# Performance work log

Hardware: AMD Instinct MI355X
Metric: run time of the kernel (lower is better)

## Reference

```python
import jax, jax.numpy as jnp
import numpy as np

B = 1; T = 2048; H = 2048; NH = 16; KVH = 4; HD = 128; WIN = 512; SINK = 64
S = 64; NG = 4; MLP_I = 5504; CK = 4
INTER = NH * HD; CONV_DIM = INTER + 2 * NG * S; NPROJ = INTER + CONV_DIM + NH
EPS = 1e-6; MEPS = 1e-5


def rmsnorm(x, w, eps):
    return x * jax.lax.rsqrt(jnp.mean(x * x, -1, keepdims=True) + eps) * w


def rotate_half(x):
    h = x.shape[-1] // 2
    return jnp.concatenate([-x[..., h:], x[..., :h]], -1)


def setup_inputs():
    key = jax.random.key(0)
    ks = jax.random.split(key, 32)
    rn = lambda k, s, sc=0.02: jax.random.normal(k, s, dtype=jnp.float32) * sc
    inv = 1.0 / (10000.0 ** (np.arange(0, HD, 2, dtype=np.float64) / HD))
    fr = np.outer(np.arange(T), inv)
    emb = np.concatenate([fr, fr], -1)
    return {
        'hidden_states': jax.random.normal(ks[0], (B, T, H), dtype=jnp.float32),
        'cos': jnp.asarray(np.cos(emb), jnp.float32)[None],
        'sin': jnp.asarray(np.sin(emb), jnp.float32)[None],
        'ln1_w': jnp.ones((H,), jnp.float32),
        'q_w': rn(ks[1], (NH * HD, H)), 'q_b': rn(ks[2], (NH * HD,)),
        'k_w': rn(ks[3], (KVH * HD, H)), 'k_b': rn(ks[4], (KVH * HD,)),
        'v_w': rn(ks[5], (KVH * HD, H)), 'v_b': rn(ks[6], (KVH * HD,)),
        'o_w': rn(ks[7], (H, NH * HD)),
        'in_proj_w': rn(ks[8], (NPROJ, H)),
        'conv_w': rn(ks[9], (CONV_DIM, 1, CK), 0.1),
        'conv_b': rn(ks[10], (CONV_DIM,), 0.1),
        'dt_bias': rn(ks[11], (NH,), 0.5),
        'A_log': rn(ks[12], (NH,), 0.5),
        'D': rn(ks[13], (NH,), 0.5),
        'mnorm_w': jnp.ones((INTER,), jnp.float32),
        'out_proj_w': rn(ks[14], (H, INTER)),
        'ln2_w': jnp.ones((H,), jnp.float32),
        'gate_w': rn(ks[15], (MLP_I, H)),
        'up_w': rn(ks[16], (MLP_I, H)),
        'down_w': rn(ks[17], (H, MLP_I)),
    }


def _mamba2(ev, in_proj_w, conv_w, conv_b, dt_bias, A_log, D, mnorm_w, out_proj_w):
    # ev: [B, L, H] evicted hidden states; Mamba2 with expand=1 (intermediate=INTER)
    L = ev.shape[1]
    proj = jnp.einsum('blh,ph->blp', ev, in_proj_w)
    z = proj[..., :INTER]
    xBC = proj[..., INTER:INTER + CONV_DIM]
    dt = proj[..., INTER + CONV_DIM:]
    # depthwise causal conv1d, kernel 4
    xBC = jax.lax.conv_general_dilated(
        xBC.transpose(0, 2, 1), conv_w, (1,), [(CK - 1, 0)],
        dimension_numbers=('NCH', 'OIH', 'NCH'), feature_group_count=CONV_DIM)
    xBC = jax.nn.silu((xBC + conv_b[None, :, None]).transpose(0, 2, 1))
    x = xBC[..., :INTER].reshape(B, L, NH, HD)
    Bm = jnp.repeat(xBC[..., INTER:INTER + NG * S].reshape(B, L, NG, S), NH // NG, axis=2)
    Cm = jnp.repeat(xBC[..., INTER + NG * S:].reshape(B, L, NG, S), NH // NG, axis=2)
    dt = jax.nn.softplus(dt + dt_bias)  # [B, L, NH]
    A = -jnp.exp(A_log)  # [NH]

    def scan_one(xb, bb, cb, db):
        def step(state, inp):
            xt, bt, ct, dtt = inp  # [NH,HD],[NH,S],[NH,S],[NH]
            decay = jnp.exp(dtt * A)[:, None, None]
            state = decay * state + (dtt[:, None] * xt)[..., None] * bt[:, None, :]
            y = jnp.einsum('hds,hs->hd', state, ct) + D[:, None] * xt
            return state, y
        _, ys = jax.lax.scan(step, jnp.zeros((NH, HD, S), xb.dtype), (xb, bb, cb, db))
        return ys

    y = jax.vmap(scan_one)(x, Bm, Cm, dt).reshape(B, L, INTER)
    g = y * jax.nn.silu(z)  # gated RMSNorm
    g = g * jax.lax.rsqrt(jnp.mean(g * g, -1, keepdims=True) + MEPS) * mnorm_w
    return jnp.einsum('bli,hi->blh', g, out_proj_w)


def reference(hidden_states, cos, sin, ln1_w, q_w, q_b, k_w, k_b, v_w, v_b, o_w,
              in_proj_w, conv_w, conv_b, dt_bias, A_log, D, mnorm_w, out_proj_w,
              ln2_w, gate_w, up_w, down_w):
    pre = rmsnorm(hidden_states, ln1_w, EPS)  # input_layernorm
    evict_end = T - WIN
    mem_out = _mamba2(pre[:, SINK:evict_end, :], in_proj_w, conv_w, conv_b,
                      dt_bias, A_log, D, mnorm_w, out_proj_w)  # [B, Le, H]
    mem_act = mem_out[:, -1:, :]

    def qkv(x, w, b, nh):
        return (jnp.einsum('blh,ph->blp', x, w) + b).reshape(x.shape[0], x.shape[1], nh, HD).transpose(0, 2, 1, 3)

    q = qkv(pre, q_w, q_b, NH)
    k = qkv(pre, k_w, k_b, KVH)
    v = qkv(pre, v_w, v_b, KVH)
    c = cos[:, None]; s = sin[:, None]
    q = q * c + rotate_half(q) * s
    k = k * c + rotate_half(k) * s
    # mem token injection at position SINK (mem projections are not rotated)
    q = q.at[:, :, SINK, :].set(qkv(mem_act, q_w, q_b, NH)[:, :, 0, :])
    k = k.at[:, :, SINK, :].set(qkv(mem_act, k_w, k_b, KVH)[:, :, 0, :])
    v = v.at[:, :, SINK, :].set(qkv(mem_act, v_w, v_b, KVH)[:, :, 0, :])
    # sink + sliding-window causal mask with mem-token bias
    row = jnp.arange(T)[:, None]; col = jnp.arange(T)[None, :]
    protected = SINK + 1
    bad = (col > row) | ((col < row - WIN) & (col >= protected))
    minv = jnp.finfo(jnp.float32).min
    mask = jnp.where(bad, minv, 0.0)[None, None]
    le_fact = (T - SINK - WIN) / T
    mask = mask.at[..., SINK].add(0.5 * le_fact)
    rep = NH // KVH
    kf = jnp.repeat(k, rep, axis=1)
    vf = jnp.repeat(v, rep, axis=1)
    scores = jnp.einsum('bhqd,bhkd->bhqk', q, kf) * (HD ** -0.5) + mask
    attn = jax.nn.softmax(scores, axis=-1)
    o = jnp.einsum('bhqk,bhkd->bhqd', attn, vf).transpose(0, 2, 1, 3).reshape(B, T, NH * HD)
    # training-path merge: sinks | mem_out | window
    merged = jnp.concatenate([o[:, :SINK], mem_out, o[:, T - WIN:]], axis=1)
    attn_out = jnp.einsum('blp,hp->blh', merged, o_w)
    h = hidden_states + attn_out
    m = rmsnorm(h, ln2_w, EPS)
    mlp = jnp.einsum('bli,hi->blh',
                     jax.nn.silu(jnp.einsum('blh,ih->bli', m, gate_w)) * jnp.einsum('blh,ih->bli', m, up_w),
                     down_w)
    return h + mlp
```

## Files before the change

### kernel.cpp

```cpp
#include <hip/hip_runtime.h>
#include <hip/hip_bf16.h>

#define TSEQ   2048
#define HDIM   2048
#define NHEAD  16
#define KVHEAD 4
#define HEADD  128
#define WINSZ  512
#define SINKN  64
#define MLPI   5504
#define CONVD  2560
#define NPROJD 4624
#define LMEM   1472
#define NCHUNK 23
#define QKVD   3072

typedef unsigned short bf_t;
typedef __attribute__((ext_vector_type(8))) short short8;
typedef __attribute__((ext_vector_type(4))) short s4v;
typedef __attribute__((ext_vector_type(4))) float ffrag;

#define BOF_PRE   0ull
#define BOF_QKV   8388608ull
#define BOF_P     8388608ull
// ... 27 lines not shown
typedef const __attribute__((address_space(1))) unsigned gl_u32;
typedef __attribute__((address_space(3))) unsigned lds_u32;
__device__ __forceinline__ void gld16(const void* g, void* l) {
  __builtin_amdgcn_global_load_lds((gl_u32*)g, (lds_u32*)l, 16, 0, 0);
}

__global__ void detect_k(const void* __restrict__ ln1, int* __restrict__ flag) {
  unsigned w0 = *(const unsigned*)ln1;
  *flag = (w0 == 0x3F803F80u) ? 1 : 0;
}

__global__ __launch_bounds__(256) void wconv_k(const float* __restrict__ src,
    bf_t* __restrict__ dst, int n8, const int* __restrict__ flagp) {
  if (*flagp) return;
  int idx = blockIdx.x*256 + threadIdx.x;
  if (idx >= n8) return;
  const float* s = src + (size_t)idx*8;
  float4 a = *(const float4*)s, b = *(const float4*)(s+4);
  short8 o;
  o[0]=(short)f2bf(a.x); o[1]=(short)f2bf(a.y); o[2]=(short)f2bf(a.z); o[3]=(short)f2bf(a.w);
  o[4]=(short)f2bf(b.x); o[5]=(short)f2bf(b.y); o[6]=(short)f2bf(b.z); o[7]=(short)f2bf(b.w);
  *(short8*)(dst + (size_t)idx*8) = o;
}

__global__ __launch_bounds__(256) void rms_in_k(const void* __restrict__ x,
    const void* __restrict__ w, bf_t* __restrict__ out, float eps,
    const int* __restrict__ flagp) {
  int bf = *flagp;
  int row = blockIdx.x, tid = threadIdx.x;
  float v[8];
  if (bf) {
    const bf_t* xr = (const bf_t*)x + (size_t)row*HDIM + tid*8;
#pragma unroll
    for (int j = 0; j < 8; ++j) v[j] = bf2f(xr[j]);
  } else {
    const float* xr = (const float*)x + (size_t)row*HDIM + tid*8;
    float4 a = *(const float4*)xr, b = *(const float4*)(xr+4);
    v[0]=a.x; v[1]=a.y; v[2]=a.z; v[3]=a.w; v[4]=b.x; v[5]=b.y; v[6]=b.z; v[7]=b.w;
  }
  float ss = 0.f;
#pragma unroll
  for (int j = 0; j < 8; ++j) ss += v[j]*v[j];
  __shared__ float red[256];
  red[tid] = ss; __syncthreads();
  for (int s = 128; s > 0; s >>= 1) { if (tid < s) red[tid] += red[tid+s]; __syncthreads(); }
  float scale = 1.f / sqrtf(red[0]*(1.f/HDIM) + eps);
  bf_t* o = out + (size_t)row*HDIM + tid*8;
#pragma unroll
  for (int j = 0; j < 8; ++j) o[j] = f2bf(v[j]*scale*ldin(w, tid*8+j, bf));
}

__global__ __launch_bounds__(256) void rms_f2b_k(const float* __restrict__ x,
    const void* __restrict__ w, bf_t* __restrict__ out, float eps,
    const int* __restrict__ flagp) {
  int bf = *flagp;
  int row = blockIdx.x, tid = threadIdx.x;
  const float* xr = x + (size_t)row*2048 + tid*8;
  float4 a = *(const float4*)xr, b = *(const float4*)(xr+4);
  float v[8] = {a.x,a.y,a.z,a.w,b.x,b.y,b.z,b.w};
  float ss = 0.f;
#pragma unroll
  for (int j = 0; j < 8; ++j) ss += v[j]*v[j];
  __shared__ float red[256];
  red[tid] = ss; __syncthreads();
  for (int s = 128; s > 0; s >>= 1) { if (tid < s) red[tid] += red[tid+s]; __syncthreads(); }
  float scale = 1.f / sqrtf(red[0]*(1.f/2048.f) + eps);
  bf_t* o = out + (size_t)row*2048 + tid*8;
#pragma unroll
  for (int j = 0; j < 8; ++j) o[j] = f2bf(v[j]*scale*ldin(w, tid*8+j, bf));
}

__global__ __launch_bounds__(256) void tgemm_k(
    const bf_t* __restrict__ A, int lda,
    const void* __restrict__ W0, const void* __restrict__ W1, const void* __restrict__ W2,
    const bf_t* __restrict__ C0, const bf_t* __restrict__ C1, const bf_t* __restrict__ C2,
    int ldw, int n1, int n2,
    const void* __restrict__ b0, const void* __restrict__ b1, const void* __restrict__ b2,
    const void* __restrict__ res,
    const float* __restrict__ hf,
    void* __restrict__ out,
    int ldc, int M, int N, int K, int mode, int outbf,
    const int* __restrict__ flagp) {
  int bf = *flagp;
  __shared__ short As[4096];
  __shared__ short Bs[2048];
  int tid = threadIdx.x;
  int lane = tid & 63, wv = tid >> 6;
  int bm = blockIdx.y << 7, bn = blockIdx.x << 6;

  int trow = tid >> 2;
  int kc = (tid & 3) << 3;
  int ar0 = bm + trow;        if (ar0 > M-1) ar0 = M-1;
  int ar1 = bm + 64 + trow;   if (ar1 > M-1) ar1 = M-1;
  int wr  = bn + trow;        if (wr > N-1) wr = N-1;
  const bf_t* ga0 = A + (size_t)ar0*lda + kc;
  const bf_t* ga1 = A + (size_t)ar1*lda + kc;
  const bf_t* w0 = bf ? (const bf_t*)W0 : C0;
  const bf_t* w1 = bf ? (const bf_t*)W1 : C1;
  const bf_t* w2 = bf ? (const bf_t*)W2 : C2;
  const bf_t* Wsel; int wrl;
  if (wr < n1)      { Wsel = w0; wrl = wr; }
  else if (wr < n2) { Wsel = w1; wrl = wr - n1; }
  else              { Wsel = w2; wrl = wr - n2; }
  const bf_t* gwb = Wsel + (size_t)wrl*ldw + kc;
  short* lA0 = As + wv*512;
  short* lA1 = As + 2048 + wv*512;
  short* lB  = Bs + wv*512;

  int wm = (wv & 1) << 6, wn = (wv >> 1) << 5;
  int fr = lane & 15, fq = (lane >> 4) << 3;

  ffrag acc[4][2];
#pragma unroll
  for (int i = 0; i < 4; ++i)
#pragma unroll
    for (int j = 0; j < 2; ++j) acc[i][j] = (ffrag){0.f,0.f,0.f,0.f};

  for (int k0 = 0; k0 < K; k0 += 32) {
    gld16(ga0 + k0, lA0);
    gld16(ga1 + k0, lA1);
    gld16(gwb + k0, lB);
    __syncthreads();
    short8 af[4], bfr[2];
#pragma unroll
    for (int i = 0; i < 4; ++i)
      af[i] = *(const short8*)&As[(wm + i*16 + fr)*32 + fq];
#pragma unroll
    for (int j = 0; j < 2; ++j)
      bfr[j] = *(const short8*)&Bs[(wn + j*16 + fr)*32 + fq];
#pragma unroll
    for (int i = 0; i < 4; ++i)
#pragma unroll
      for (int j = 0; j < 2; ++j)
        acc[i][j] = __builtin_amdgcn_mfma_f32_16x16x32_bf16(af[i], bfr[j], acc[i][j], 0, 0, 0);
    __syncthreads();
  }

  int rbase = (lane >> 4) << 2;
  int cbase = lane & 15;
#pragma unroll
  for (int i = 0; i < 4; ++i) {
#pragma unroll
    for (int j = 0; j < 2; ++j) {
#pragma unroll
      for (int r = 0; r < 4; ++r) {
        int m = bm + wm + i*16 + rbase + r;
        int n = bn + wn + j*16 + cbase;
        if (m >= M || n >= N) continue;
        size_t ci = (size_t)m*ldc + n;
        float v = acc[i][j][r];
        if (mode == 0) {
          if (b0) {
            if (n < n1)      v += ldin(b0, n, bf);
            else if (n < n2) v += ldin(b1, n - n1, bf);
            else             v += ldin(b2, n - n2, bf);
          }
          if (outbf) ((bf_t*)out)[ci] = f2bf(v); else ((float*)out)[ci] = v;
        } else if (mode == 1) {
          ((float*)out)[ci] = v + ldin(res, ci, bf);
        } else {
          float hv = hf[ci] + v;
          if (bf) ((bf_t*)out)[ci] = f2bf(hv); else ((float*)out)[ci] = hv;
        }
      }
    }
  }
}

__global__ __launch_bounds__(256) void fgemm_k(
    const bf_t* __restrict__ A, int lda,
    const void* __restrict__ Wg, const void* __restrict__ Wu,
    const bf_t* __restrict__ Cg, const bf_t* __restrict__ Cu, int ldw,
    bf_t* __restrict__ out, int M, int N, int K,
    const int* __restrict__ flagp) {
  int bf = *flagp;
  __shared__ short As[4096];
  __shared__ short Bs[4096];
  int tid = threadIdx.x;
  int lane = tid & 63, wv = tid >> 6;
  int bm = blockIdx.y << 7, bn = blockIdx.x << 6;

  int trow = tid >> 2;
  int kc = (tid & 3) << 3;
  int ar0 = bm + trow;        if (ar0 > M-1) ar0 = M-1;
  int ar1 = bm + 64 + trow;   if (ar1 > M-1) ar1 = M-1;
  int wr  = bn + trow;        if (wr > N-1) wr = N-1;
  const bf_t* ga0 = A + (size_t)ar0*lda + kc;
  const bf_t* ga1 = A + (size_t)ar1*lda + kc;
  const bf_t* wg = bf ? (const bf_t*)Wg : Cg;
  const bf_t* wu = bf ? (const bf_t*)Wu : Cu;
  const bf_t* gwgb = wg + (size_t)wr*ldw + kc;
  const bf_t* gwub = wu + (size_t)wr*ldw + kc;
  short* lA0 = As + wv*512;
  short* lA1 = As + 2048 + wv*512;
  short* lBg = Bs + wv*512;
  short* lBu = Bs + 2048 + wv*512;

  int wm = (wv & 1) << 6, wn = (wv >> 1) << 5;
  int fr = lane & 15, fq = (lane >> 4) << 3;

  ffrag ag[4][2], au[4][2];
#pragma unroll
  for (int i = 0; i < 4; ++i)
#pragma unroll
    for (int j = 0; j < 2; ++j) { ag[i][j] = (ffrag){0.f,0.f,0.f,0.f}; au[i][j] = (ffrag){0.f,0.f,0.f,0.f}; }

  for (int k0 = 0; k0 < K; k0 += 32) {
    gld16(ga0 + k0, lA0);
    gld16(ga1 + k0, lA1);
    gld16(gwgb + k0, lBg);
    gld16(gwub + k0, lBu);
    __syncthreads();
    short8 af[4], bg[2], bu[2];
#pragma unroll
    for (int i = 0; i < 4; ++i)
      af[i] = *(const short8*)&As[(wm + i*16 + fr)*32 + fq];
#pragma unroll
    for (int j = 0; j < 2; ++j) {
      bg[j] = *(const short8*)&Bs[(wn + j*16 + fr)*32 + fq];
      bu[j] = *(const short8*)&Bs[2048 + (wn + j*16 + fr)*32 + fq];
    }
#pragma unroll
    for (int i = 0; i < 4; ++i)
#pragma unroll
      for (int j = 0; j < 2; ++j) {
        ag[i][j] = __builtin_amdgcn_mfma_f32_16x16x32_bf16(af[i], bg[j], ag[i][j], 0, 0, 0);
        au[i][j] = __builtin_amdgcn_mfma_f32_16x16x32_bf16(af[i], bu[j], au[i][j], 0, 0, 0);
      }
    __syncthreads();
  }

  int rbase = (lane >> 4) << 2;
  int cbase = lane & 15;
#pragma unroll
  for (int i = 0; i < 4; ++i)
#pragma unroll
    for (int j = 0; j < 2; ++j)
#pragma unroll
      for (int r = 0; r < 4; ++r) {
        int m = bm + wm + i*16 + rbase + r;
        int n = bn + wn + j*16 + cbase;
        if (m >= M || n >= N) continue;
        float g = ag[i][j][r], u = au[i][j][r];
        out[(size_t)m*N + n] = f2bf(siluf(g) * u);
      }
}

__global__ __launch_bounds__(256) void rope_k(float* __restrict__ tb, int stride,
    const void* __restrict__ cosp, const void* __restrict__ sinp,
    int nheads, const int* __restrict__ flagp) {
  int bf = *flagp;
  int idx = blockIdx.x*256 + threadIdx.x;
  int d = idx & 63;
  int rem = idx >> 6;
  int tpos = rem / nheads, hh = rem % nheads;
  float* base = tb + (size_t)tpos*stride + hh*128;
  float a = base[d], b = base[d+64];
  float c0 = ldin(cosp, (size_t)tpos*128 + d, bf),    s0 = ldin(sinp, (size_t)tpos*128 + d, bf);
  float c1 = ldin(cosp, (size_t)tpos*128 + d + 64, bf), s1 = ldin(sinp, (size_t)tpos*128 + d + 64, bf);
  base[d]    = a*c0 - b*s0;
  base[d+64] = b*c1 + a*s1;
}

__global__ __launch_bounds__(256) void conv_k(const float* __restrict__ proj,
    const void* __restrict__ convw, const void* __restrict__ convb,
    float* __restrict__ xbcc, const int* __restrict__ flagp) {
  int bf = *flagp;
  int idx = blockIdx.x*256 + threadIdx.x;
  int t = idx / CONVD, c = idx % CONVD;
  float acc = ldin(convb, c, bf);
#pragma unroll
  for (int j = 0; j < 4; ++j) {
    int tt = t - 3 + j;
    if (tt >= 0) acc += ldin(convw, (size_t)c*4 + j, bf) * proj[(size_t)tt*NPROJD + 2048 + c];
  }
  xbcc[idx] = siluf(acc);
}

__global__ __launch_bounds__(256) void dt_k(const float* __restrict__ proj,
    const void* __restrict__ dtb, const void* __restrict__ alog,
    float* __restrict__ dtv, float* __restrict__ ga, const int* __restrict__ flagp) {
  int bf = *flagp;
  int idx = blockIdx.x*256 + threadIdx.x;
  int t = idx >> 4, h = idx & 15;
  float raw = proj[(size_t)t*NPROJD + 4608 + h] + ldin(dtb, h, bf);
  float dt = (raw > 30.f) ? raw : log1pf(expf(raw));
  float A = -expf(ldin(alog, h, bf));
  dtv[idx] = dt;
  ga[idx] = dt*A;
}

__global__ __launch_bounds__(256) void cums_k(const float* __restrict__ ga,
    float* __restrict__ Lc) {
  int wid = blockIdx.x*4 + (threadIdx.x >> 6);
  int lane = threadIdx.x & 63;
  int h = wid / NCHUNK, c = wid % NCHUNK;
  int t = c*64 + lane;
  float a = ga[(size_t)t*16 + h];
#pragma unroll
  for (int off = 1; off < 64; off <<= 1) {
    float o = __shfl_up(a, off, 64);
    if (lane >= off) a += o;
  }
  Lc[(size_t)(h*NCHUNK + c)*64 + lane] = a;
}

__global__ __launch_bounds__(256) void chunkstate_k(
    const float* __restrict__ xbcc, const float* __restrict__ dtv,
    const float* __restrict__ Lc, float* __restrict__ Pbuf) {
  __shared__ short XT[128*72];
  __shared__ short BT[64*72];
  __shared__ float wj[64];
  int tid = threadIdx.x, lane = tid & 63, wv = tid >> 6;
  int b = blockIdx.x;
  int h = b & 15, c = b >> 4;
  int g64 = (h >> 2) << 6;
  size_t hc = (size_t)(h*NCHUNK + c);

  if (tid < 64) {
    float L63 = Lc[hc*64 + 63];
// ... 129 lines not shown
    }
  }
  __syncthreads();

  {
    int rbase = (lane >> 4) << 2, cbase = lane & 15;
    int j = wv*16 + cbase;
#pragma unroll
    for (int i = 0; i < 4; ++i)
#pragma unroll
      for (int r = 0; r < 4; ++r) {
        int ii = i*16 + rbase + r;
        float v = (j <= ii) ? s0[i][r] * expf(Lch[ii] - Lch[j]) * dtch[j] : 0.f;
        BsS[ii*72 + j] = (short)f2bf(v);
      }
#pragma unroll
    for (int e = 0; e < 16; ++e) {
      int idx = tid*16 + e;
      int ii = idx >> 6, s = idx & 63;
      Cs[ii*72 + s] = (short)f2bf(bf2f((bf_t)Cs[ii*72 + s]) * expf(Lch[ii]));
    }
  }
  __syncthreads();

  ffrag acc[4][2];
#pragma unroll
  for (int i = 0; i < 4; ++i)
#pragma unroll
    for (int j = 0; j < 2; ++j) acc[i][j] = (ffrag){0.f,0.f,0.f,0.f};
#pragma unroll
  for (int k0 = 0; k0 < 64; k0 += 32) {
    short8 xb[2], af[4];
#pragma unroll
    for (int j = 0; j < 2; ++j)
      xb[j] = *(const short8*)&XT[(wv*32 + j*16 + fr)*72 + k0 + fq];
#pragma unroll
    for (int i = 0; i < 4; ++i)
      af[i] = *(const short8*)&BsS[(i*16 + fr)*72 + k0 + fq];
#pragma unroll
    for (int i = 0; i < 4; ++i)
#pragma unroll
      for (int j = 0; j < 2; ++j)
        acc[i][j] = __builtin_amdgcn_mfma_f32_16x16x32_bf16(af[i], xb[j], acc[i][j], 0, 0, 0);
  }
#pragma unroll
  for (int k0 = 0; k0 < 64; k0 += 32) {
    short8 sb[2], af[4];
#pragma unroll
    for (int j = 0; j < 2; ++j)
      sb[j] = *(const short8*)&Sinb[(wv*32 + j*16 + fr)*72 + k0 + fq];
#pragma unroll
    for (int i = 0; i < 4; ++i)
      af[i] = *(const short8*)&Cs[(i*16 + fr)*72 + k0 + fq];
#pragma unroll
    for (int i = 0; i < 4; ++i)
#pragma unroll
      for (int j = 0; j < 2; ++j)
        acc[i][j] = __builtin_amdgcn_mfma_f32_16x16x32_bf16(af[i], sb[j], acc[i][j], 0, 0, 0);
  }

  int rbase = (lane >> 4) << 2, cbase = lane & 15;
#pragma unroll
  for (int i = 0; i < 4; ++i)
#pragma unroll
    for (int j = 0; j < 2; ++j)
#pragma unroll
      for (int r = 0; r < 4; ++r) {
        int ii = i*16 + rbase + r;
        int d = wv*32 + j*16 + cbase;
        int t = c*64 + ii;
        int col = h*128 + d;
        float x = xbcc[(size_t)t*CONVD + col];
        float z = proj[(size_t)t*NPROJD + col];
        float y = acc[i][j][r] + Dh*x;
        g[(size_t)t*2048 + col] = y * siluf(z);
      }
}

__global__ __launch_bounds__(256) void memact_k(
    const bf_t* __restrict__ merged,
    const void* __restrict__ qw, const void* __restrict__ qb,
    const void* __restrict__ kw, const void* __restrict__ kb,
    const void* __restrict__ vw, const void* __restrict__ vb,
    float* __restrict__ qkv, const int* __restrict__ flagp) {
  int bf = *flagp;
  int p = blockIdx.x, tid = threadIdx.x;
  const bf_t* ma = merged + (size_t)1535*2048;
  const void* w; const void* b; int off;
  if (p < 2048)      { w = qw; b = qb; off = p; }
  else if (p < 2560) { w = kw; b = kb; off = p - 2048; }
  else               { w = vw; b = vb; off = p - 2560; }
  float partial = 0.f;
  size_t wbase = (size_t)off*2048;
  for (int j = tid; j < 2048; j += 256) partial += bf2f(ma[j])*ldin(w, wbase + j, bf);
  __shared__ float red[256];
  red[tid] = partial; __syncthreads();
  for (int s = 128; s > 0; s >>= 1) { if (tid < s) red[tid] += red[tid+s]; __syncthreads(); }
  if (tid == 0) qkv[(size_t)64*QKVD + p] = red[0] + ldin(b, off, bf);
}

__global__ __launch_bounds__(256) void attn3_k(
    const float* __restrict__ qkv, bf_t* __restrict__ merged) {
  __shared__ short Qs[64*136];
  __shared__ short Ks[64*136];
  __shared__ short Vt[128*72];
  __shared__ short Pb[64*72];

  int bid = blockIdx.x;
  int g = bid & 3, hg = (bid >> 2) & 3, qt = bid >> 4;
  int r0 = (qt == 0) ? 0 : (1536 + 64*(qt-1));
  int tid = threadIdx.x, lane = tid & 63, wv = tid >> 6;

  int qcol = g*512 + hg*128;
  int kcol = 2048 + g*128;
  int vcol = 2560 + g*128;

  int fr = lane & 15, fq = (lane >> 4) << 3;
  int rloc = (lane >> 4) << 2;
  int cb = lane & 15;

  {
    int row = tid >> 2, c4 = tid & 3;
    const float* qp = qkv + (size_t)(r0 + row)*QKVD + qcol;
#pragma unroll
    for (int rep = 0; rep < 8; ++rep) {
      int d = (c4 + rep*4)*4;
      float4 v = *(const float4*)(qp + d);
      s4v o;
      o[0] = (short)f2bf(v.x); o[1] = (short)f2bf(v.y);
      o[2] = (short)f2bf(v.z); o[3] = (short)f2bf(v.w);
      *(s4v*)&Qs[row*136 + d] = o;
    }
  }
  __syncthreads();

  float m4[4] = {-3.0e38f, -3.0e38f, -3.0e38f, -3.0e38f};
  float l4[4] = {0.f, 0.f, 0.f, 0.f};
  ffrag o8[8];
#pragma unroll
  for (int n = 0; n < 8; ++n) o8[n] = (ffrag){0.f,0.f,0.f,0.f};

  int ntiles = (qt == 0) ? 1 : 11;
  for (int t = 0; t < ntiles; ++t) {
    int kb = (t == 0) ? 0 : ((t == 1) ? 64 : (r0 - 512 + 64*(t-2)));

    {
      int row = tid >> 2, c4 = tid & 3;
      const float* kp = qkv + (size_t)(kb + row)*QKVD + kcol;
#pragma unroll
      for (int rep = 0; rep < 8; ++rep) {
        int d = (c4 + rep*4)*4;
        float4 v = *(const float4*)(kp + d);
        s4v o;
        o[0] = (short)f2bf(v.x); o[1] = (short)f2bf(v.y);
        o[2] = (short)f2bf(v.z); o[3] = (short)f2bf(v.w);
        *(s4v*)&Ks[row*136 + d] = o;
      }
    }
#pragma unroll
    for (int it = 0; it < 8; ++it) {
      int task = tid + it*256;
      int d = task & 127, jg = task >> 7;
      const float* vp = qkv + (size_t)(kb + jg*4)*QKVD + vcol + d;
      s4v o;
      o[0] = (short)f2bf(vp[0]);
      o[1] = (short)f2bf(vp[QKVD]);
      o[2] = (short)f2bf(vp[2*QKVD]);
      o[3] = (short)f2bf(vp[3*QKVD]);
      *(s4v*)&Vt[d*72 + jg*4] = o;
    }
    __syncthreads();

    ffrag s[4];
#pragma unroll
    for (int n = 0; n < 4; ++n) s[n] = (ffrag){0.f,0.f,0.f,0.f};
#pragma unroll
    for (int k0 = 0; k0 < 128; k0 += 32) {
// ... 41 lines not shown
#pragma unroll
      for (int rg = 0; rg < 4; ++rg) {
        float p = expf(s[n][rg] - m4[rg]);
        ts[rg] += p;
        Pb[(wv*16 + rloc + rg)*72 + n*16 + cb] = (short)f2bf(p);
      }
#pragma unroll
    for (int rg = 0; rg < 4; ++rg) {
#pragma unroll
      for (int off = 1; off < 16; off <<= 1) ts[rg] += __shfl_xor(ts[rg], off, 64);
      l4[rg] += ts[rg];
    }

#pragma unroll
    for (int k0 = 0; k0 < 64; k0 += 32) {
      short8 ap = *(const short8*)&Pb[(wv*16 + fr)*72 + k0 + fq];
#pragma unroll
      for (int n = 0; n < 8; ++n) {
        short8 bv = *(const short8*)&Vt[(n*16 + fr)*72 + k0 + fq];
        o8[n] = __builtin_amdgcn_mfma_f32_16x16x32_bf16(ap, bv, o8[n], 0, 0, 0);
      }
    }
    __syncthreads();
  }

  float inv[4];
#pragma unroll
  for (int rg = 0; rg < 4; ++rg) inv[rg] = 1.f / l4[rg];
#pragma unroll
  for (int n = 0; n < 8; ++n)
#pragma unroll
    for (int rg = 0; rg < 4; ++rg) {
      int i = wv*16 + rloc + rg;
      int d = n*16 + cb;
      merged[(size_t)(r0 + i)*2048 + (g*4 + hg)*128 + d] = f2bf(o8[n][rg]*inv[rg]);
    }
}

extern "C" void kernel_launch(void* const* d_in, const int* in_sizes, int n_in,
                              void* d_out, int out_size, void* d_ws, size_t ws_size,
                              hipStream_t stream) {
  const void* hidden = d_in[0];
  const void* cosp   = d_in[1];
  const void* sinp   = d_in[2];
  const void* ln1w   = d_in[3];
  const void* qw = d_in[4];  const void* qb = d_in[5];
  const void* kw = d_in[6];  const void* kb = d_in[7];
  const void* vw = d_in[8];  const void* vb = d_in[9];
  const void* ow = d_in[10];
  const void* inpw = d_in[11];
  const void* convw = d_in[12]; const void* convb = d_in[13];
  const void* dtb = d_in[14]; const void* alog = d_in[15]; const void* dd = d_in[16];
  const void* mnw = d_in[17]; const void* outpw = d_in[18];
  const void* ln2w = d_in[19];
  const void* gatew = d_in[20]; const void* upw = d_in[21]; const void* downw = d_in[22];

  char* wsb = (char*)d_ws;
  bf_t*  pre    = (bf_t*)(wsb + BOF_PRE);
  bf_t*  mbuf   = (bf_t*)(wsb + BOF_PRE);
  float* qkv    = (float*)(wsb + BOF_QKV);
  float* Pbuf   = (float*)(wsb + BOF_P);
  float* Sbuf   = (float*)(wsb + BOF_S);
  float* proj   = (float*)(wsb + BOF_PROJ);
  bf_t*  Gbuf   = (bf_t*)(wsb + BOF_GB);
  float* xbcc   = (float*)(wsb + BOF_XBCC);
  float* gbuf   = (float*)(wsb + BOF_GF);
  bf_t*  merged = (bf_t*)(wsb + BOF_MERG);
  bf_t*  gn     = (bf_t*)(wsb + BOF_GN);
  float* hbuf   = (float*)(wsb + BOF_H);
  float* dtv    = (float*)(wsb + BOF_DT);
  float* ga     = (float*)(wsb + BOF_GA);
  int*   flag   = (int*)(wsb + BOF_FLAG);
  float* Lc     = (float*)(wsb + BOF_LC);
  bf_t*  cvA    = (bf_t*)(wsb + BOF_CNV_A);
  bf_t*  cvB    = (bf_t*)(wsb + BOF_CNV_B);
  bf_t*  cvq    = cvB;
  bf_t*  cvk    = cvB + 4194304;
  bf_t*  cvv    = cvB + 5242880;

  detect_k<<<dim3(1), dim3(1), 0, stream>>>(ln1w, flag);
  rms_in_k<<<dim3(TSEQ), dim3(256), 0, stream>>>(hidden, ln1w, pre, 1e-6f, flag);

  wconv_k<<<dim3(4624), dim3(256), 0, stream>>>((const float*)inpw, cvA, 1183744, flag);
  tgemm_k<<<dim3(73,12), dim3(256), 0, stream>>>(pre + (size_t)64*2048, 2048,
      inpw, nullptr, nullptr, cvA, nullptr, nullptr, 2048, NPROJD, NPROJD,
      nullptr, nullptr, nullptr,
      nullptr, nullptr, proj, NPROJD, LMEM, NPROJD, 2048, 0, 0, flag);
  conv_k<<<dim3((LMEM*CONVD)/256), dim3(256), 0, stream>>>(proj, convw, convb, xbcc, flag);
  dt_k<<<dim3((LMEM*16)/256), dim3(256), 0, stream>>>(proj, dtb, alog, dtv, ga, flag);
  cums_k<<<dim3(92), dim3(256), 0, stream>>>(ga, Lc);
  chunkstate_k<<<dim3(368), dim3(256), 0, stream>>>(xbcc, dtv, Lc, Pbuf);
  statepass_k<<<dim3(512), dim3(256), 0, stream>>>(Pbuf, Lc, Sbuf);
  wconv_k<<<dim3(2048), dim3(256), 0, stream>>>((const float*)outpw, cvA, 524288, flag);
  chunkout_k<<<dim3(368), dim3(256), 0, stream>>>(xbcc, proj, dtv, Lc, Sbuf, dd, gbuf, flag);
  rms_f2b_k<<<dim3(LMEM), dim3(256), 0, stream>>>(gbuf, mnw, gn, 1e-5f, flag);
  tgemm_k<<<dim3(32,12), dim3(256), 0, stream>>>(gn, 2048,
      outpw, nullptr, nullptr, cvA, nullptr, nullptr, 2048, 2048, 2048,
      nullptr, nullptr, nullptr,
      nullptr, nullptr, merged + (size_t)64*2048, 2048, LMEM, 2048, 2048, 0, 1, flag);

  wconv_k<<<dim3(2048), dim3(256), 0, stream>>>((const float*)qw, cvq, 524288, flag);
  wconv_k<<<dim3(512),  dim3(256), 0, stream>>>((const float*)kw, cvk, 131072, flag);
  wconv_k<<<dim3(512),  dim3(256), 0, stream>>>((const float*)vw, cvv, 131072, flag);
  tgemm_k<<<dim3(48,16), dim3(256), 0, stream>>>(pre, 2048,
      qw, kw, vw, cvq, cvk, cvv, 2048, 2048, 2560, qb, kb, vb,
      nullptr, nullptr, qkv, QKVD, 2048, QKVD, 2048, 0, 0, flag);
  rope_k<<<dim3(8192), dim3(256), 0, stream>>>(qkv, QKVD, cosp, sinp, 16, flag);
  rope_k<<<dim3(2048), dim3(256), 0, stream>>>(qkv + 2048, QKVD, cosp, sinp, 4, flag);

  memact_k<<<dim3(3072), dim3(256), 0, stream>>>(merged, qw, qb, kw, kb, vw, vb, qkv, flag);
  attn3_k<<<dim3(144), dim3(256), 0, stream>>>(qkv, merged);

  wconv_k<<<dim3(2048), dim3(256), 0, stream>>>((const float*)ow, cvB, 524288, flag);
  tgemm_k<<<dim3(32,16), dim3(256), 0, stream>>>(merged, 2048,
      ow, nullptr, nullptr, cvB, nullptr, nullptr, 2048, 2048, 2048,
      nullptr, nullptr, nullptr,
      hidden, nullptr, hbuf, 2048, 2048, 2048, 2048, 1, 0, flag);
  rms_f2b_k<<<dim3(TSEQ), dim3(256), 0, stream>>>(hbuf, ln2w, mbuf, 1e-6f, flag);

  wconv_k<<<dim3(5504), dim3(256), 0, stream>>>((const float*)gatew, cvA, 1409024, flag);
  wconv_k<<<dim3(5504), dim3(256), 0, stream>>>((const float*)upw,   cvB, 1409024, flag);
  fgemm_k<<<dim3(86,16), dim3(256), 0, stream>>>(mbuf, 2048, gatew, upw, cvA, cvB, 2048,
      Gbuf, 2048, MLPI, 2048, flag);
  wconv_k<<<dim3(5504), dim3(256), 0, stream>>>((const float*)downw, cvA, 1409024, flag);
  tgemm_k<<<dim3(32,16), dim3(256), 0, stream>>>(Gbuf, MLPI,
      downw, nullptr, nullptr, cvA, nullptr, nullptr, MLPI, 2048, 2048,
      nullptr, nullptr, nullptr,
      nullptr, hbuf, d_out, 2048, 2048, 2048, MLPI, 3, 0, flag);
}
```

Baseline: 705.0 us.

## Enlarge GEMM tiles to 128x128 and 128x96 and use bf16 weights in memact

The generic GEMM's block tile grows from 128x64 to 128x128, with each wave computing a 64x64 sub-tile (4x4 MFMA fragments). The fused gate/up GEMM grows to 128x96 per block. Grid sizes shrink to match. The goal is more reuse of each loaded tile per K step and less redundant global traffic for the A operand. memact_k now reads the pre-converted bf16 weight copies instead of converting fp32 weights on the fly. The trade-offs are higher register and LDS use, lower occupancy, and fewer blocks on the smaller GEMMs, which may underfill the 256 CUs.

Measured after the change: 785.8 us. +11.5%, slower.

```diff
diff --git a/kernel.cpp b/kernel.cpp
--- a/kernel.cpp
+++ b/kernel.cpp
@@ -134,55 +134,65 @@
     const int* __restrict__ flagp) {
   int bf = *flagp;
   __shared__ short As[4096];
-  __shared__ short Bs[2048];
+  __shared__ short Bs[4096];
   int tid = threadIdx.x;
   int lane = tid & 63, wv = tid >> 6;
-  int bm = blockIdx.y << 7, bn = blockIdx.x << 6;
+  int bm = blockIdx.y << 7, bn = blockIdx.x << 7;
 
   int trow = tid >> 2;
   int kc = (tid & 3) << 3;
   int ar0 = bm + trow;        if (ar0 > M-1) ar0 = M-1;
   int ar1 = bm + 64 + trow;   if (ar1 > M-1) ar1 = M-1;
-  int wr  = bn + trow;        if (wr > N-1) wr = N-1;
+  int wr0 = bn + trow;        if (wr0 > N-1) wr0 = N-1;
+  int wr1 = bn + 64 + trow;   if (wr1 > N-1) wr1 = N-1;
   const bf_t* ga0 = A + (size_t)ar0*lda + kc;
   const bf_t* ga1 = A + (size_t)ar1*lda + kc;
   const bf_t* w0 = bf ? (const bf_t*)W0 : C0;
   const bf_t* w1 = bf ? (const bf_t*)W1 : C1;
   const bf_t* w2 = bf ? (const bf_t*)W2 : C2;
-  const bf_t* Wsel; int wrl;
-  if (wr < n1)      { Wsel = w0; wrl = wr; }
-  else if (wr < n2) { Wsel = w1; wrl = wr - n1; }
-  else              { Wsel = w2; wrl = wr - n2; }
-  const bf_t* gwb = Wsel + (size_t)wrl*ldw + kc;
+  const bf_t* gwb0; const bf_t* gwb1;
+  {
+    const bf_t* Ws; int wrl;
+    if (wr0 < n1)      { Ws = w0; wrl = wr0; }
+    else if (wr0 < n2) { Ws = w1; wrl = wr0 - n1; }
+    else               { Ws = w2; wrl = wr0 - n2; }
+    gwb0 = Ws + (size_t)wrl*ldw + kc;
+    if (wr1 < n1)      { Ws = w0; wrl = wr1; }
+    else if (wr1 < n2) { Ws = w1; wrl = wr1 - n1; }
+    else               { Ws = w2; wrl = wr1 - n2; }
+    gwb1 = Ws + (size_t)wrl*ldw + kc;
+  }
   short* lA0 = As + wv*512;
   short* lA1 = As + 2048 + wv*512;
-  short* lB  = Bs + wv*512;
-
-  int wm = (wv & 1) << 6, wn = (wv >> 1) << 5;
+  short* lB0 = Bs + wv*512;
+  short* lB1 = Bs + 2048 + wv*512;
+
+  int wm = (wv & 1) << 6, wn = (wv >> 1) << 6;
   int fr = lane & 15, fq = (lane >> 4) << 3;
 
-  ffrag acc[4][2];
+  ffrag acc[4][4];
 #pragma unroll
   for (int i = 0; i < 4; ++i)
 #pragma unroll
-    for (int j = 0; j < 2; ++j) acc[i][j] = (ffrag){0.f,0.f,0.f,0.f};
+    for (int j = 0; j < 4; ++j) acc[i][j] = (ffrag){0.f,0.f,0.f,0.f};
 
   for (int k0 = 0; k0 < K; k0 += 32) {
     gld16(ga0 + k0, lA0);
     gld16(ga1 + k0, lA1);
-    gld16(gwb + k0, lB);
+    gld16(gwb0 + k0, lB0);
+    gld16(gwb1 + k0, lB1);
     __syncthreads();
-    short8 af[4], bfr[2];
+    short8 af[4], bfr[4];
 #pragma unroll
     for (int i = 0; i < 4; ++i)
       af[i] = *(const short8*)&As[(wm + i*16 + fr)*32 + fq];
 #pragma unroll
-    for (int j = 0; j < 2; ++j)
+    for (int j = 0; j < 4; ++j)
       bfr[j] = *(const short8*)&Bs[(wn + j*16 + fr)*32 + fq];
 #pragma unroll
     for (int i = 0; i < 4; ++i)
 #pragma unroll
-      for (int j = 0; j < 2; ++j)
+      for (int j = 0; j < 4; ++j)
         acc[i][j] = __builtin_amdgcn_mfma_f32_16x16x32_bf16(af[i], bfr[j], acc[i][j], 0, 0, 0);
     __syncthreads();
   }
@@ -192,7 +202,7 @@
 #pragma unroll
   for (int i = 0; i < 4; ++i) {
 #pragma unroll
-    for (int j = 0; j < 2; ++j) {
+    for (int j = 0; j < 4; ++j) {
 #pragma unroll
       for (int r = 0; r < 4; ++r) {
         int m = bm + wm + i*16 + rbase + r;
@@ -226,55 +236,63 @@
     const int* __restrict__ flagp) {
   int bf = *flagp;
   __shared__ short As[4096];
-  __shared__ short Bs[4096];
+  __shared__ short Bs[6144];
   int tid = threadIdx.x;
   int lane = tid & 63, wv = tid >> 6;
-  int bm = blockIdx.y << 7, bn = blockIdx.x << 6;
+  int bm = blockIdx.y << 7, bn = blockIdx.x * 96;
 
   int trow = tid >> 2;
   int kc = (tid & 3) << 3;
   int ar0 = bm + trow;        if (ar0 > M-1) ar0 = M-1;
   int ar1 = bm + 64 + trow;   if (ar1 > M-1) ar1 = M-1;
-  int wr  = bn + trow;        if (wr > N-1) wr = N-1;
   const bf_t* ga0 = A + (size_t)ar0*lda + kc;
   const bf_t* ga1 = A + (size_t)ar1*lda + kc;
   const bf_t* wg = bf ? (const bf_t*)Wg : Cg;
   const bf_t* wu = bf ? (const bf_t*)Wu : Cu;
-  const bf_t* gwgb = wg + (size_t)wr*ldw + kc;
-  const bf_t* gwub = wu + (size_t)wr*ldw + kc;
+  const bf_t* gbsrc[3];
+#pragma unroll
+  for (int p = 0; p < 3; ++p) {
+    int g = p*256 + tid;
+    int isu = (g >= 384);
+    int r = isu ? ((g - 384) >> 2) : (g >> 2);
+    int col = bn + r; if (col > N-1) col = N-1;
+    gbsrc[p] = (isu ? wu : wg) + (size_t)col*ldw + ((g & 3) << 3);
+  }
   short* lA0 = As + wv*512;
   short* lA1 = As + 2048 + wv*512;
-  short* lBg = Bs + wv*512;
-  short* lBu = Bs + 2048 + wv*512;
-
-  int wm = (wv & 1) << 6, wn = (wv >> 1) << 5;
+  short* lBp0 = Bs + wv*512;
+  short* lBp1 = Bs + 2048 + wv*512;
+  short* lBp2 = Bs + 4096 + wv*512;
+
+  int wm = (wv & 1) << 6, wn = (wv >> 1) * 48;
   int fr = lane & 15, fq = (lane >> 4) << 3;
 
-  ffrag ag[4][2], au[4][2];
+  ffrag ag[4][3], au[4][3];
 #pragma unroll
   for (int i = 0; i < 4; ++i)
 #pragma unroll
-    for (int j = 0; j < 2; ++j) { ag[i][j] = (ffrag){0.f,0.f,0.f,0.f}; au[i][j] = (ffrag){0.f,0.f,0.f,0.f}; }
+    for (int j = 0; j < 3; ++j) { ag[i][j] = (ffrag){0.f,0.f,0.f,0.f}; au[i][j] = (ffrag){0.f,0.f,0.f,0.f}; }
 
   for (int k0 = 0; k0 < K; k0 += 32) {
     gld16(ga0 + k0, lA0);
     gld16(ga1 + k0, lA1);
-    gld16(gwgb + k0, lBg);
-    gld16(gwub + k0, lBu);
+    gld16(gbsrc[0] + k0, lBp0);
+    gld16(gbsrc[1] + k0, lBp1);
+    gld16(gbsrc[2] + k0, lBp2);
     __syncthreads();
-    short8 af[4], bg[2], bu[2];
+    short8 af[4], bg[3], bu[3];
 #pragma unroll
     for (int i = 0; i < 4; ++i)
       af[i] = *(const short8*)&As[(wm + i*16 + fr)*32 + fq];
 #pragma unroll
-    for (int j = 0; j < 2; ++j) {
+    for (int j = 0; j < 3; ++j) {
       bg[j] = *(const short8*)&Bs[(wn + j*16 + fr)*32 + fq];
-      bu[j] = *(const short8*)&Bs[2048 + (wn + j*16 + fr)*32 + fq];
+      bu[j] = *(const short8*)&Bs[3072 + (wn + j*16 + fr)*32 + fq];
     }
 #pragma unroll
     for (int i = 0; i < 4; ++i)
 #pragma unroll
-      for (int j = 0; j < 2; ++j) {
+      for (int j = 0; j < 3; ++j) {
         ag[i][j] = __builtin_amdgcn_mfma_f32_16x16x32_bf16(af[i], bg[j], ag[i][j], 0, 0, 0);
         au[i][j] = __builtin_amdgcn_mfma_f32_16x16x32_bf16(af[i], bu[j], au[i][j], 0, 0, 0);
       }
@@ -286,7 +304,7 @@
 #pragma unroll
   for (int i = 0; i < 4; ++i)
 #pragma unroll
-    for (int j = 0; j < 2; ++j)
+    for (int j = 0; j < 3; ++j)
 #pragma unroll
       for (int r = 0; r < 4; ++r) {
         int m = bm + wm + i*16 + rbase + r;
@@ -582,17 +600,18 @@
     const void* __restrict__ qw, const void* __restrict__ qb,
     const void* __restrict__ kw, const void* __restrict__ kb,
     const void* __restrict__ vw, const void* __restrict__ vb,
+    const bf_t* __restrict__ cq, const bf_t* __restrict__ ck, const bf_t* __restrict__ cv,
     float* __restrict__ qkv, const int* __restrict__ flagp) {
   int bf = *flagp;
   int p = blockIdx.x, tid = threadIdx.x;
   const bf_t* ma = merged + (size_t)1535*2048;
-  const void* w; const void* b; int off;
-  if (p < 2048)      { w = qw; b = qb; off = p; }
-  else if (p < 2560) { w = kw; b = kb; off = p - 2048; }
-  else               { w = vw; b = vb; off = p - 2560; }
+  const void* b; const bf_t* wb; int off;
+  if (p < 2048)      { wb = bf ? (const bf_t*)qw : cq; b = qb; off = p; }
+  else if (p < 2560) { wb = bf ? (const bf_t*)kw : ck; b = kb; off = p - 2048; }
+  else               { wb = bf ? (const bf_t*)vw : cv; b = vb; off = p - 2560; }
   float partial = 0.f;
   size_t wbase = (size_t)off*2048;
-  for (int j = tid; j < 2048; j += 256) partial += bf2f(ma[j])*ldin(w, wbase + j, bf);
+  for (int j = tid; j < 2048; j += 256) partial += bf2f(ma[j])*bf2f(wb[wbase + j]);
   __shared__ float red[256];
   red[tid] = partial; __syncthreads();
   for (int s = 128; s > 0; s >>= 1) { if (tid < s) red[tid] += red[tid+s]; __syncthreads(); }
@@ -800,7 +819,7 @@
   rms_in_k<<<dim3(TSEQ), dim3(256), 0, stream>>>(hidden, ln1w, pre, 1e-6f, flag);
 
   wconv_k<<<dim3(4624), dim3(256), 0, stream>>>((const float*)inpw, cvA, 1183744, flag);
-  tgemm_k<<<dim3(73,12), dim3(256), 0, stream>>>(pre + (size_t)64*2048, 2048,
+  tgemm_k<<<dim3(37,12), dim3(256), 0, stream>>>(pre + (size_t)64*2048, 2048,
       inpw, nullptr, nullptr, cvA, nullptr, nullptr, 2048, NPROJD, NPROJD,
       nullptr, nullptr, nullptr,
       nullptr, nullptr, proj, NPROJD, LMEM, NPROJD, 2048, 0, 0, flag);
@@ -812,7 +831,7 @@
   wconv_k<<<dim3(2048), dim3(256), 0, stream>>>((const float*)outpw, cvA, 524288, flag);
   chunkout_k<<<dim3(368), dim3(256), 0, stream>>>(xbcc, proj, dtv, Lc, Sbuf, dd, gbuf, flag);
   rms_f2b_k<<<dim3(LMEM), dim3(256), 0, stream>>>(gbuf, mnw, gn, 1e-5f, flag);
-  tgemm_k<<<dim3(32,12), dim3(256), 0, stream>>>(gn, 2048,
+  tgemm_k<<<dim3(16,12), dim3(256), 0, stream>>>(gn, 2048,
       outpw, nullptr, nullptr, cvA, nullptr, nullptr, 2048, 2048, 2048,
       nullptr, nullptr, nullptr,
       nullptr, nullptr, merged + (size_t)64*2048, 2048, LMEM, 2048, 2048, 0, 1, flag);
@@ -820,17 +839,18 @@
   wconv_k<<<dim3(2048), dim3(256), 0, stream>>>((const float*)qw, cvq, 524288, flag);
   wconv_k<<<dim3(512),  dim3(256), 0, stream>>>((const float*)kw, cvk, 131072, flag);
   wconv_k<<<dim3(512),  dim3(256), 0, stream>>>((const float*)vw, cvv, 131072, flag);
-  tgemm_k<<<dim3(48,16), dim3(256), 0, stream>>>(pre, 2048,
+  tgemm_k<<<dim3(24,16), dim3(256), 0, stream>>>(pre, 2048,
       qw, kw, vw, cvq, cvk, cvv, 2048, 2048, 2560, qb, kb, vb,
       nullptr, nullptr, qkv, QKVD, 2048, QKVD, 2048, 0, 0, flag);
   rope_k<<<dim3(8192), dim3(256), 0, stream>>>(qkv, QKVD, cosp, sinp, 16, flag);
   rope_k<<<dim3(2048), dim3(256), 0, stream>>>(qkv + 2048, QKVD, cosp, sinp, 4, flag);
 
-  memact_k<<<dim3(3072), dim3(256), 0, stream>>>(merged, qw, qb, kw, kb, vw, vb, qkv, flag);
+  memact_k<<<dim3(3072), dim3(256), 0, stream>>>(merged, qw, qb, kw, kb, vw, vb,
+      cvq, cvk, cvv, qkv, flag);
   attn3_k<<<dim3(144), dim3(256), 0, stream>>>(qkv, merged);
 
   wconv_k<<<dim3(2048), dim3(256), 0, stream>>>((const float*)ow, cvB, 524288, flag);
-  tgemm_k<<<dim3(32,16), dim3(256), 0, stream>>>(merged, 2048,
+  tgemm_k<<<dim3(16,16), dim3(256), 0, stream>>>(merged, 2048,
       ow, nullptr, nullptr, cvB, nullptr, nullptr, 2048, 2048, 2048,
       nullptr, nullptr, nullptr,
       hidden, nullptr, hbuf, 2048, 2048, 2048, 2048, 1, 0, flag);
@@ -838,10 +858,10 @@
 
   wconv_k<<<dim3(5504), dim3(256), 0, stream>>>((const float*)gatew, cvA, 1409024, flag);
   wconv_k<<<dim3(5504), dim3(256), 0, stream>>>((const float*)upw,   cvB, 1409024, flag);
-  fgemm_k<<<dim3(86,16), dim3(256), 0, stream>>>(mbuf, 2048, gatew, upw, cvA, cvB, 2048,
+  fgemm_k<<<dim3(58,16), dim3(256), 0, stream>>>(mbuf, 2048, gatew, upw, cvA, cvB, 2048,
       Gbuf, 2048, MLPI, 2048, flag);
   wconv_k<<<dim3(5504), dim3(256), 0, stream>>>((const float*)downw, cvA, 1409024, flag);
-  tgemm_k<<<dim3(32,16), dim3(256), 0, stream>>>(Gbuf, MLPI,
+  tgemm_k<<<dim3(16,16), dim3(256), 0, stream>>>(Gbuf, MLPI,
       downw, nullptr, nullptr, cvA, nullptr, nullptr, MLPI, 2048, 2048,
       nullptr, nullptr, nullptr,
       nullptr, hbuf, d_out, 2048, 2048, 2048, MLPI, 3, 0, flag);
```

## Double-buffer LDS tiles in GEMM kernels and read pre-converted bf16 weights in memact

Applied to the files above, without the earlier changes.

Both tiled GEMM kernels (tgemm_k and fgemm_k) now use two LDS buffers. Each iteration issues the next k-slice's global-to-LDS loads before computing on the current buffer, which drops one barrier per iteration and lets loads overlap MFMA work. The cost is twice the shared memory per block, which can lower occupancy. memact_k now reads the already-converted bf16 q/k/v weight copies, where it previously did fp32 loads with per-element conversion, cutting its memory traffic.

After: 669.3 us. 1.05x faster.

```diff
diff --git a/kernel.cpp b/kernel.cpp
--- a/kernel.cpp
+++ b/kernel.cpp
@@ -133,8 +133,8 @@
     int ldc, int M, int N, int K, int mode, int outbf,
     const int* __restrict__ flagp) {
   int bf = *flagp;
-  __shared__ short As[4096];
-  __shared__ short Bs[2048];
+  __shared__ short As[8192];
+  __shared__ short Bs[4096];
   int tid = threadIdx.x;
   int lane = tid & 63, wv = tid >> 6;
   int bm = blockIdx.y << 7, bn = blockIdx.x << 6;
@@ -154,9 +154,7 @@
   else if (wr < n2) { Wsel = w1; wrl = wr - n1; }
   else              { Wsel = w2; wrl = wr - n2; }
   const bf_t* gwb = Wsel + (size_t)wrl*ldw + kc;
-  short* lA0 = As + wv*512;
-  short* lA1 = As + 2048 + wv*512;
-  short* lB  = Bs + wv*512;
+  int sA = wv*512;
 
   int wm = (wv & 1) << 6, wn = (wv >> 1) << 5;
   int fr = lane & 15, fq = (lane >> 4) << 3;
@@ -167,24 +165,36 @@
 #pragma unroll
     for (int j = 0; j < 2; ++j) acc[i][j] = (ffrag){0.f,0.f,0.f,0.f};
 
+  gld16(ga0, As + sA);
+  gld16(ga1, As + 2048 + sA);
+  gld16(gwb, Bs + sA);
+  __syncthreads();
+
+  int cur = 0;
   for (int k0 = 0; k0 < K; k0 += 32) {
-    gld16(ga0 + k0, lA0);
-    gld16(ga1 + k0, lA1);
-    gld16(gwb + k0, lB);
-    __syncthreads();
+    int nxt = k0 + 32;
+    int nb = (cur ^ 1) << 12;
+    int nbB = (cur ^ 1) << 11;
+    if (nxt < K) {
+      gld16(ga0 + nxt, As + nb + sA);
+      gld16(ga1 + nxt, As + nb + 2048 + sA);
+      gld16(gwb + nxt, Bs + nbB + sA);
+    }
+    int cbA = cur << 12, cbB = cur << 11;
     short8 af[4], bfr[2];
 #pragma unroll
     for (int i = 0; i < 4; ++i)
-      af[i] = *(const short8*)&As[(wm + i*16 + fr)*32 + fq];
+      af[i] = *(const short8*)&As[cbA + (wm + i*16 + fr)*32 + fq];
 #pragma unroll
     for (int j = 0; j < 2; ++j)
-      bfr[j] = *(const short8*)&Bs[(wn + j*16 + fr)*32 + fq];
+      bfr[j] = *(const short8*)&Bs[cbB + (wn + j*16 + fr)*32 + fq];
 #pragma unroll
     for (int i = 0; i < 4; ++i)
 #pragma unroll
       for (int j = 0; j < 2; ++j)
         acc[i][j] = __builtin_amdgcn_mfma_f32_16x16x32_bf16(af[i], bfr[j], acc[i][j], 0, 0, 0);
     __syncthreads();
+    cur ^= 1;
   }
 
   int rbase = (lane >> 4) << 2;
@@ -225,8 +235,8 @@
     bf_t* __restrict__ out, int M, int N, int K,
     const int* __restrict__ flagp) {
   int bf = *flagp;
-  __shared__ short As[4096];
-  __shared__ short Bs[4096];
+  __shared__ short As[8192];
+  __shared__ short Bs[8192];
   int tid = threadIdx.x;
   int lane = tid & 63, wv = tid >> 6;
   int bm = blockIdx.y << 7, bn = blockIdx.x << 6;
@@ -242,10 +252,7 @@
   const bf_t* wu = bf ? (const bf_t*)Wu : Cu;
   const bf_t* gwgb = wg + (size_t)wr*ldw + kc;
   const bf_t* gwub = wu + (size_t)wr*ldw + kc;
-  short* lA0 = As + wv*512;
-  short* lA1 = As + 2048 + wv*512;
-  short* lBg = Bs + wv*512;
-  short* lBu = Bs + 2048 + wv*512;
+  int sA = wv*512;
 
   int wm = (wv & 1) << 6, wn = (wv >> 1) << 5;
   int fr = lane & 15, fq = (lane >> 4) << 3;
@@ -256,20 +263,31 @@
 #pragma unroll
     for (int j = 0; j < 2; ++j) { ag[i][j] = (ffrag){0.f,0.f,0.f,0.f}; au[i][j] = (ffrag){0.f,0.f,0.f,0.f}; }
 
+  gld16(ga0, As + sA);
+  gld16(ga1, As + 2048 + sA);
+  gld16(gwgb, Bs + sA);
+  gld16(gwub, Bs + 2048 + sA);
+  __syncthreads();
+
+  int cur = 0;
   for (int k0 = 0; k0 < K; k0 += 32) {
-    gld16(ga0 + k0, lA0);
-    gld16(ga1 + k0, lA1);
-    gld16(gwgb + k0, lBg);
-    gld16(gwub + k0, lBu);
-    __syncthreads();
+    int nxt = k0 + 32;
+    int nb = (cur ^ 1) << 12;
+    if (nxt < K) {
+      gld16(ga0 + nxt, As + nb + sA);
+      gld16(ga1 + nxt, As + nb + 2048 + sA);
+      gld16(gwgb + nxt, Bs + nb + sA);
+      gld16(gwub + nxt, Bs + nb + 2048 + sA);
+    }
+    int cb = cur << 12;
     short8 af[4], bg[2], bu[2];
 #pragma unroll
     for (int i = 0; i < 4; ++i)
-      af[i] = *(const short8*)&As[(wm + i*16 + fr)*32 + fq];
+      af[i] = *(const short8*)&As[cb + (wm + i*16 + fr)*32 + fq];
 #pragma unroll
     for (int j = 0; j < 2; ++j) {
-      bg[j] = *(const short8*)&Bs[(wn + j*16 + fr)*32 + fq];
-      bu[j] = *(const short8*)&Bs[2048 + (wn + j*16 + fr)*32 + fq];
+      bg[j] = *(const short8*)&Bs[cb + (wn + j*16 + fr)*32 + fq];
+      bu[j] = *(const short8*)&Bs[cb + 2048 + (wn + j*16 + fr)*32 + fq];
     }
 #pragma unroll
     for (int i = 0; i < 4; ++i)
@@ -279,6 +297,7 @@
         au[i][j] = __builtin_amdgcn_mfma_f32_16x16x32_bf16(af[i], bu[j], au[i][j], 0, 0, 0);
       }
     __syncthreads();
+    cur ^= 1;
   }
 
   int rbase = (lane >> 4) << 2;
@@ -582,17 +601,18 @@
     const void* __restrict__ qw, const void* __restrict__ qb,
     const void* __restrict__ kw, const void* __restrict__ kb,
     const void* __restrict__ vw, const void* __restrict__ vb,
+    const bf_t* __restrict__ cq, const bf_t* __restrict__ ck, const bf_t* __restrict__ cv,
     float* __restrict__ qkv, const int* __restrict__ flagp) {
   int bf = *flagp;
   int p = blockIdx.x, tid = threadIdx.x;
   const bf_t* ma = merged + (size_t)1535*2048;
-  const void* w; const void* b; int off;
-  if (p < 2048)      { w = qw; b = qb; off = p; }
-  else if (p < 2560) { w = kw; b = kb; off = p - 2048; }
-  else               { w = vw; b = vb; off = p - 2560; }
+  const void* b; const bf_t* wb; int off;
+  if (p < 2048)      { wb = bf ? (const bf_t*)qw : cq; b = qb; off = p; }
+  else if (p < 2560) { wb = bf ? (const bf_t*)kw : ck; b = kb; off = p - 2048; }
+  else               { wb = bf ? (const bf_t*)vw : cv; b = vb; off = p - 2560; }
   float partial = 0.f;
   size_t wbase = (size_t)off*2048;
-  for (int j = tid; j < 2048; j += 256) partial += bf2f(ma[j])*ldin(w, wbase + j, bf);
+  for (int j = tid; j < 2048; j += 256) partial += bf2f(ma[j])*bf2f(wb[wbase + j]);
   __shared__ float red[256];
   red[tid] = partial; __syncthreads();
   for (int s = 128; s > 0; s >>= 1) { if (tid < s) red[tid] += red[tid+s]; __syncthreads(); }
@@ -826,7 +846,8 @@
   rope_k<<<dim3(8192), dim3(256), 0, stream>>>(qkv, QKVD, cosp, sinp, 16, flag);
   rope_k<<<dim3(2048), dim3(256), 0, stream>>>(qkv + 2048, QKVD, cosp, sinp, 4, flag);
 
-  memact_k<<<dim3(3072), dim3(256), 0, stream>>>(merged, qw, qb, kw, kb, vw, vb, qkv, flag);
+  memact_k<<<dim3(3072), dim3(256), 0, stream>>>(merged, qw, qb, kw, kb, vw, vb,
+      cvq, cvk, cvv, qkv, flag);
   attn3_k<<<dim3(144), dim3(256), 0, stream>>>(qkv, merged);
 
   wconv_k<<<dim3(2048), dim3(256), 0, stream>>>((const float*)ow, cvB, 524288, flag);
```
